# Kernel optimization log

Hardware: AMD Instinct MI355X
Metric: run time of the kernel (lower is better)

## Reference

```python
import jax, jax.numpy as jnp
import numpy as np

N = 50000
E = 800000
DIN = 256
DH = 256
DOUT = 256
R = 8
B = 4


def setup_inputs() -> dict:
    key = jax.random.key(0)
    ks = jax.random.split(key, 12)
    s = 0.05
    return {
        "x": jax.random.normal(ks[0], (N, DIN), jnp.float32),
        "edge_index": jax.random.randint(ks[1], (2, E), 0, N, jnp.int64),
        "edge_type": jax.random.randint(ks[2], (E,), 0, R, jnp.int64),
        "basis1": jax.random.normal(ks[3], (B, DIN, DH), jnp.float32) * s,
        "comp1": jax.random.normal(ks[4], (R, B), jnp.float32) * s,
        "root1": jax.random.normal(ks[5], (DIN, DH), jnp.float32) * s,
        "bias1": jnp.zeros((DH,), jnp.float32),
        "basis2": jax.random.normal(ks[6], (B, DH, DOUT), jnp.float32) * s,
        "comp2": jax.random.normal(ks[7], (R, B), jnp.float32) * s,
        "root2": jax.random.normal(ks[8], (DH, DOUT), jnp.float32) * s,
        "bias2": jnp.zeros((DOUT,), jnp.float32),
    }


def rgcn_conv(x, src, dst, edge_type, basis, comp, root, bias):
    # Basis-decomposed relational conv (PyG RGCNConv, aggr='mean').
    # xb: per-node transform by each basis matrix -> [N, B, out]
    xb = jnp.einsum('ni,bio->nbo', x, basis)
    # Per-edge message: mix bases with relation coefficients -> [E, out]
    msg = jnp.einsum('eb,ebo->eo', comp[edge_type], xb[src])
    # Mean aggregation per (dst, relation): divide each edge by the count of
    # edges of its relation arriving at its destination, then scatter-add.
    key = dst * R + edge_type
    cnt = jax.ops.segment_sum(jnp.ones((msg.shape[0],), x.dtype), key,
                              num_segments=x.shape[0] * R)
    norm = 1.0 / jnp.maximum(cnt, 1.0)
    agg = jax.ops.segment_sum(msg * norm[key][:, None], dst,
                              num_segments=x.shape[0])
    return agg + x @ root + bias


def reference(x, edge_index, edge_type, basis1, comp1, root1, bias1,
              basis2, comp2, root2, bias2):
    src, dst = edge_index[0], edge_index[1]
    h = rgcn_conv(x, src, dst, edge_type, basis1, comp1, root1, bias1)
    h = jax.nn.relu(h)
    # dropout(p=0.4) is identity in eval mode
    out = rgcn_conv(h, src, dst, edge_type, basis2, comp2, root2, bias2)
    return out
```

## Files before the change

### kernel.cpp

```cpp
#include <hip/hip_runtime.h>
#include <hip/hip_bf16.h>

constexpr int N_NODES = 50000;
constexpr int N_EDGES = 800000;
constexpr int R_REL   = 8;
constexpr int BASES   = 4;
constexpr int D       = 256;
constexpr int KZ      = BASES * D;
constexpr int KT      = KZ + D;
constexpr int WSTRIDE = 16;
constexpr int DUMMY_P = 8 << 20;

constexpr int NHI    = (N_NODES + 255) / 256;
constexpr int NS_BLK = 200;
constexpr int CH     = N_EDGES / NS_BLK;

constexpr int CB4 = (N_NODES * 128) / 1024;
constexpr int WKB = KT / 64;
constexpr int CAP = N_EDGES + N_NODES * 8;
constexpr int FB4 = (CAP + 1023) / 1024;

typedef __attribute__((ext_vector_type(8))) short bf16x8;
typedef __attribute__((ext_vector_type(4))) float f32x4;

__device__ inline float bfu_lo(unsigned u) { return __uint_as_float(u << 16); }
__device__ inline float bfu_hi(unsigned u) { return __uint_as_float(u & 0xFFFF0000u); }
__device__ inline unsigned short f2bu(float f) {
  __hip_bfloat16 h = __float2bfloat16(f);
  return *reinterpret_cast<unsigned short*>(&h);
}
__device__ inline void store_out(float* p, float v) { *p = v; }
__device__ inline void store_out(__hip_bfloat16* p, float v) { *p = __float2bfloat16(v); }

__device__ inline void gload_lds16(void* lds, const void* g) {
  __builtin_amdgcn_global_load_lds(
      (const __attribute__((address_space(1))) unsigned*)g,
      (__attribute__((address_space(3))) unsigned*)lds, 16, 0, 0);
}

__global__ __launch_bounds__(256) void prep_kernel(
    const int* __restrict__ ei, const int* __restrict__ et,
    int* __restrict__ gcoarse,
    const float* __restrict__ x, unsigned* __restrict__ x2,
    const float* __restrict__ basis1, const float* __restrict__ root1,
    __hip_bfloat16* __restrict__ WT1,
    const float* __restrict__ basis2, const float* __restrict__ root2,
    __hip_bfloat16* __restrict__ WT2,
    int* __restrict__ packed) {
  __shared__ __hip_bfloat16 tile[16][256];
  __shared__ int hist[NHI];
  int bid = blockIdx.x;
  int tid = threadIdx.x;

  if (bid < NS_BLK) {
    if (tid < NHI) hist[tid] = 0;
    __syncthreads();
    int start = bid * CH, end = start + CH;
    for (int i = start + tid; i < end; i += 256) {
      int dst = ei[N_EDGES + i];
      atomicAdd(&hist[dst >> 8], 1);
    }
    __syncthreads();
    if (tid < NHI && hist[tid] > 0) atomicAdd(&gcoarse[tid], hist[tid]);
    return;
  }
  bid -= NS_BLK;
  if (bid < CB4) {
    int idx = (bid * 256 + tid) * 4;
    const float* px = x + (size_t)idx * 2;
    float4 a = *(const float4*)(px);
    float4 b = *(const float4*)(px + 4);
    uint4 o;
    o.x = (unsigned)f2bu(a.x) | ((unsigned)f2bu(a.y) << 16);
    o.y = (unsigned)f2bu(a.z) | ((unsigned)f2bu(a.w) << 16);
    o.z = (unsigned)f2bu(b.x) | ((unsigned)f2bu(b.y) << 16);
    o.w = (unsigned)f2bu(b.z) | ((unsigned)f2bu(b.w) << 16);
    *(uint4*)(x2 + idx) = o;
    return;
  }
  bid -= CB4;
  if (bid < 2 * WKB) {
    const float* basis = (bid < WKB) ? basis1 : basis2;
    const float* root  = (bid < WKB) ? root1 : root2;
    __hip_bfloat16* WT = (bid < WKB) ? WT1 : WT2;
    int wb = (bid < WKB) ? bid : bid - WKB;
    int k0 = wb * 64;
#pragma unroll
    for (int pass = 0; pass < 4; pass++) {
      int kp = k0 + pass * 16;
#pragma unroll
      for (int r = 0; r < 16; r++) {
        int k = kp + r;
        const float* srow = (k < KZ)
            ? basis + ((size_t)(k & 3) * D + (k >> 2)) * D
            : root + (size_t)(k - KZ) * D;
        tile[r][tid] = __float2bfloat16(srow[tid]);
      }
      __syncthreads();
      __hip_bfloat16* dst = WT + (size_t)tid * KT + kp;
#pragma unroll
      for (int c = 0; c < 2; c++) {
        union { short s[8]; int4 v; } u;
#pragma unroll
        for (int r = 0; r < 8; r++)
          u.s[r] = *reinterpret_cast<short*>(&tile[c * 8 + r][tid]);
        *(int4*)(dst + c * 8) = u.v;
      }
      __syncthreads();
    }
    return;
  }
  bid -= 2 * WKB;
  {
    int i = (bid * 256 + tid) * 4;
    if (i < CAP) {
      int4 f = make_int4(DUMMY_P, DUMMY_P, DUMMY_P, DUMMY_P);
      *(int4*)(packed + i) = f;
    }
  }
}

__global__ __launch_bounds__(256) void coarse_prefix_kernel(
    const int* __restrict__ gcoarse, int* __restrict__ gbase,
    int* __restrict__ gcur) {
  __shared__ int sd[256];
  int tid = threadIdx.x;
  int v = (tid < NHI) ? gcoarse[tid] : 0;
  sd[tid] = v;
  __syncthreads();
  for (int off = 1; off < 256; off <<= 1) {
    int t = (tid >= off) ? sd[tid - off] : 0;
    __syncthreads();
    sd[tid] += t;
    __syncthreads();
  }
  if (tid < NHI) {
    int b = sd[tid] - v;
    gbase[tid] = b;
    gcur[tid] = b;
  }
}

__global__ __launch_bounds__(256) void coarse_scatter_kernel(
    const int* __restrict__ ei, const int* __restrict__ et,
    int* __restrict__ gcur, int* __restrict__ coarse) {
  __shared__ int hist[NHI];
  __shared__ int lbase[NHI];
  __shared__ int lcnt[NHI];
  int bid = blockIdx.x;
  int tid = threadIdx.x;
  if (tid < NHI) { hist[tid] = 0; lcnt[tid] = 0; }
  __syncthreads();
  int start = bid * CH, end = start + CH;
  for (int i = start + tid; i < end; i += 256)
    atomicAdd(&hist[ei[N_EDGES + i] >> 8], 1);
  __syncthreads();
  if (tid < NHI) lbase[tid] = atomicAdd(&gcur[tid], hist[tid]);
  __syncthreads();
  for (int i = start + tid; i < end; i += 256) {
    int src = ei[i];
    int dst = ei[N_EDGES + i];
    int rt  = et[i];
    int bin = dst >> 8;
    int rank = atomicAdd(&lcnt[bin], 1);
    coarse[lbase[bin] + rank] = src | (rt << 16) | ((dst & 255) << 19);
  }
}

__global__ __launch_bounds__(256) void fine_hist_kernel(
    const int* __restrict__ coarse, const int* __restrict__ gbase,
    const int* __restrict__ gcoarse,
    const float* __restrict__ comp1, float4* __restrict__ wtab1,
    const float* __restrict__ comp2, float4* __restrict__ wtab2,
    int* __restrict__ lestart, int* __restrict__ btot) {
  __shared__ int c2[256 * R_REL];
  __shared__ int sd[256];
  int b = blockIdx.x;
  int tid = threadIdx.x;
#pragma unroll
  for (int k = tid; k < 256 * R_REL; k += 256) c2[k] = 0;
  __syncthreads();
  int base = gbase[b], n_e = gcoarse[b];
  for (int i = tid; i < n_e; i += 256) {
    int e = coarse[base + i];
    int key = ((e >> 19) & 255) * R_REL + ((e >> 16) & 7);
    atomicAdd(&c2[key], 1);
  }
  __syncthreads();
  int nodebase = b * 256;
  for (int k = tid; k < 256 * WSTRIDE; k += 256) {
    int lo = k >> 4, r = k & (WSTRIDE - 1);
    int n = nodebase + lo;
    if (n < N_NODES) {
      float4 w1 = make_float4(0.f, 0.f, 0.f, 0.f);
      float4 w2 = w1;
      if (r < R_REL) {
        int c = c2[lo * R_REL + r];
        float inv = 1.0f / (float)(c > 0 ? c : 1);
        w1.x = comp1[r * BASES + 0] * inv;
        w1.y = comp1[r * BASES + 1] * inv;
        w1.z = comp1[r * BASES + 2] * inv;
        w1.w = comp1[r * BASES + 3] * inv;
        w2.x = comp2[r * BASES + 0] * inv;
        w2.y = comp2[r * BASES + 1] * inv;
        w2.z = comp2[r * BASES + 2] * inv;
        w2.w = comp2[r * BASES + 3] * inv;
      }
      wtab1[(size_t)n * WSTRIDE + r] = w1;
      wtab2[(size_t)n * WSTRIDE + r] = w2;
    }
  }
  int d = 0;
#pragma unroll
  for (int r = 0; r < R_REL; r++) d += c2[tid * R_REL + r];
  int dp = (d + 7) & ~7;
  sd[tid] = dp;
  __syncthreads();
  for (int off = 1; off < 256; off <<= 1) {
    int t = (tid >= off) ? sd[tid - off] : 0;
    __syncthreads();
    sd[tid] += t;
    __syncthreads();
  }
  lestart[b * 256 + tid] = sd[tid] - dp;
  if (tid == 255) btot[b] = sd[255];
}

__global__ __launch_bounds__(256) void btot_prefix_kernel(
    const int* __restrict__ btot, int* __restrict__ bbase,
    int* __restrict__ estart) {
  __shared__ int sd[256];
  int tid = threadIdx.x;
  int v = (tid < NHI) ? btot[tid] : 0;
  sd[tid] = v;
  __syncthreads();
  for (int off = 1; off < 256; off <<= 1) {
    int t = (tid >= off) ? sd[tid - off] : 0;
    __syncthreads();
    sd[tid] += t;
    __syncthreads();
  }
  if (tid < NHI) bbase[tid] = sd[tid] - v;
  if (tid == NHI - 1) estart[N_NODES] = sd[tid];
}

__global__ __launch_bounds__(256) void fine_scatter_kernel(
    const int* __restrict__ coarse, const int* __restrict__ gbase,
    const int* __restrict__ gcoarse, const int* __restrict__ bbase,
    const int* __restrict__ lestart, int* __restrict__ estart,
    int* __restrict__ packed) {
  __shared__ int lest[256];
  __shared__ int lcur[256];
  int b = blockIdx.x;
  int tid = threadIdx.x;
  int sb = bbase[b];
  lest[tid] = lestart[b * 256 + tid];
  lcur[tid] = 0;
  {
    int n = b * 256 + tid;
    if (n < N_NODES) estart[n] = sb + lest[tid];
  }
  __syncthreads();
  int base = gbase[b], n_e = gcoarse[b];
  for (int i = tid; i < n_e; i += 256) {
    int e = coarse[base + i];
    int lo = (e >> 19) & 255;
    int rank = atomicAdd(&lcur[lo], 1);
    packed[sb + lest[lo] + rank] = (e & 0xFFFF) | (((e >> 16) & 7) << 20);
  }
}

__device__ inline float2 pfma(float s, float2 a, float2 c) {
  c.x = fmaf(s, a.x, c.x);
  c.y = fmaf(s, a.y, c.y);
  return c;
}

__device__ inline void edge_fma(float2 acc[BASES][2], uint2 v, float4 w) {
  float2 a01 = make_float2(bfu_lo(v.x), bfu_hi(v.x));
  float2 a23 = make_float2(bfu_lo(v.y), bfu_hi(v.y));
  acc[0][0] = pfma(w.x, a01, acc[0][0]); acc[0][1] = pfma(w.x, a23, acc[0][1]);
  acc[1][0] = pfma(w.y, a01, acc[1][0]); acc[1][1] = pfma(w.y, a23, acc[1][1]);
  acc[2][0] = pfma(w.z, a01, acc[2][0]); acc[2][1] = pfma(w.z, a23, acc[2][1]);
  acc[3][0] = pfma(w.w, a01, acc[3][0]); acc[3][1] = pfma(w.w, a23, acc[3][1]);
}

__global__ __launch_bounds__(256) void aggregate_kernel(
    const unsigned* __restrict__ x2,
    const int* __restrict__ packed,
    const int* __restrict__ estart,
    const float4* __restrict__ wtab,
    __hip_bfloat16* __restrict__ zA)
{
  int tid = threadIdx.x;
  int lane = tid & 63;
  int n = __builtin_amdgcn_readfirstlane(blockIdx.x * 4 + (tid >> 6));
  int s = __builtin_amdgcn_readfirstlane(estart[n]);
  int e = __builtin_amdgcn_readfirstlane(estart[n + 1]);
  const int voff = lane * 2;
  const float4* wt = wtab + (size_t)n * WSTRIDE;

  float2 acc[BASES][2] = {};

  for (int base = s; base < e; base += 8) {
    int4 q0 = *(const int4*)(packed + base);
    int4 q1 = *(const int4*)(packed + base + 4);
    int p0 = __builtin_amdgcn_readfirstlane(q0.x);
    int p1 = __builtin_amdgcn_readfirstlane(q0.y);
    int p2 = __builtin_amdgcn_readfirstlane(q0.z);
    int p3 = __builtin_amdgcn_readfirstlane(q0.w);
    int p4 = __builtin_amdgcn_readfirstlane(q1.x);
    int p5 = __builtin_amdgcn_readfirstlane(q1.y);
    int p6 = __builtin_amdgcn_readfirstlane(q1.z);
    int p7 = __builtin_amdgcn_readfirstlane(q1.w);
    const unsigned* r0 = x2 + ((size_t)(p0 & 0xFFFFF) << 7);
    const unsigned* r1 = x2 + ((size_t)(p1 & 0xFFFFF) << 7);
    const unsigned* r2 = x2 + ((size_t)(p2 & 0xFFFFF) << 7);
    const unsigned* r3 = x2 + ((size_t)(p3 & 0xFFFFF) << 7);
    const unsigned* r4 = x2 + ((size_t)(p4 & 0xFFFFF) << 7);
    const unsigned* r5 = x2 + ((size_t)(p5 & 0xFFFFF) << 7);
    const unsigned* r6 = x2 + ((size_t)(p6 & 0xFFFFF) << 7);
    const unsigned* r7 = x2 + ((size_t)(p7 & 0xFFFFF) << 7);
    uint2 v0 = *(const uint2*)(r0 + voff);
    uint2 v1 = *(const uint2*)(r1 + voff);
    uint2 v2 = *(const uint2*)(r2 + voff);
    uint2 v3 = *(const uint2*)(r3 + voff);
    uint2 v4 = *(const uint2*)(r4 + voff);
    uint2 v5 = *(const uint2*)(r5 + voff);
    uint2 v6 = *(const uint2*)(r6 + voff);
    uint2 v7 = *(const uint2*)(r7 + voff);
    float4 w0 = wt[p0 >> 20];
    float4 w1 = wt[p1 >> 20];
    float4 w2 = wt[p2 >> 20];
    float4 w3 = wt[p3 >> 20];
    float4 w4 = wt[p4 >> 20];
    float4 w5 = wt[p5 >> 20];
    float4 w6 = wt[p6 >> 20];
    float4 w7 = wt[p7 >> 20];
    edge_fma(acc, v0, w0);
    edge_fma(acc, v1, w1);
    edge_fma(acc, v2, w2);
    edge_fma(acc, v3, w3);
    edge_fma(acc, v4, w4);
    edge_fma(acc, v5, w5);
    edge_fma(acc, v6, w6);
    edge_fma(acc, v7, w7);
  }

  union { short s[8]; int4 v; } u0, u1;
#pragma unroll
  for (int b = 0; b < BASES; b++) {
    u0.s[b]     = (short)f2bu(acc[b][0].x);
    u0.s[4 + b] = (short)f2bu(acc[b][0].y);
    u1.s[b]     = (short)f2bu(acc[b][1].x);
    u1.s[4 + b] = (short)f2bu(acc[b][1].y);
  }
  __hip_bfloat16* zrow = zA + (size_t)n * KZ;
  *(int4*)(zrow + 16 * lane) = u0.v;
  *(int4*)(zrow + 16 * lane + 8) = u1.v;
}

#define BM 128
#define BN 256
#define BK 32

template <bool RELU, typename OutT>
__global__ __launch_bounds__(512) void gemm_kernel(
    const __hip_bfloat16* __restrict__ Az,
    const __hip_bfloat16* __restrict__ Aself,
    const __hip_bfloat16* __restrict__ Bt,
    const float* __restrict__ bias, OutT* __restrict__ C, int M) {
  __shared__ __align__(16) __hip_bfloat16 As[2][BM * BK];
  __shared__ __align__(16) __hip_bfloat16 Bs[2][BN * BK];
  int tid = threadIdx.x;
  int m0 = blockIdx.x * BM;
  int wave = tid >> 6, lane = tid & 63;
  int wm = wave & 1, wn = wave >> 1;
  int l15 = lane & 15, quad = lane >> 4;

  int colS = (lane & 3) * 8;
  int rowA = wave * 16 + (lane >> 2);
  int grA  = min(m0 + rowA, M - 1);
  const __hip_bfloat16* gAz = Az + (size_t)grA * KZ + colS;
  const __hip_bfloat16* gAs = Aself + (size_t)grA * D + colS;
  const __hip_bfloat16* gB0 = Bt + (size_t)(wave * 32 + (lane >> 2)) * KT + colS;
  const __hip_bfloat16* gB1 = gB0 + 16 * KT;

  f32x4 acc[4][4] = {};

  auto stage = [&](int buf, int k0) {
    const __hip_bfloat16* srcA = (k0 < KZ) ? (gAz + k0) : (gAs + (k0 - KZ));
    gload_lds16(As[buf] + wave * 512, srcA);
    gload_lds16(Bs[buf] + wave * 1024, gB0 + k0);
    gload_lds16(Bs[buf] + wave * 1024 + 512, gB1 + k0);
  };

  stage(0, 0);
  int cur = 0;
  for (int k0 = 0; k0 < KT; k0 += BK) {
    if (k0 + BK < KT) {
      stage(cur ^ 1, k0 + BK);
      asm volatile("s_waitcnt vmcnt(3)" ::: "memory");
    } else {
      asm volatile("s_waitcnt vmcnt(0)" ::: "memory");
    }
    __builtin_amdgcn_s_barrier();
    __builtin_amdgcn_sched_barrier(0);

    bf16x8 af[4], bfr[4];
#pragma unroll
    for (int mt = 0; mt < 4; mt++)
      af[mt] = *(const bf16x8*)(As[cur] + (wm * 64 + mt * 16 + l15) * BK + quad * 8);
#pragma unroll
    for (int nt = 0; nt < 4; nt++)
      bfr[nt] = *(const bf16x8*)(Bs[cur] + (wn * 64 + nt * 16 + l15) * BK + quad * 8);
#pragma unroll
    for (int mt = 0; mt < 4; mt++)
#pragma unroll
      for (int nt = 0; nt < 4; nt++)
        acc[mt][nt] = __builtin_amdgcn_mfma_f32_16x16x32_bf16(
            af[mt], bfr[nt], acc[mt][nt], 0, 0, 0);
    __builtin_amdgcn_s_barrier();
    cur ^= 1;
  }

#pragma unroll
  for (int nt = 0; nt < 4; nt++) {
    int cg = wn * 64 + nt * 16 + l15;
    float bv = bias[cg];
#pragma unroll
    for (int mt = 0; mt < 4; mt++) {
#pragma unroll
      for (int r = 0; r < 4; r++) {
        int rg = m0 + wm * 64 + mt * 16 + quad * 4 + r;
        if (rg < M) {
          float v = acc[mt][nt][r] + bv;
          if (RELU) v = fmaxf(v, 0.f);
          store_out(C + (size_t)rg * D + cg, v);
        }
      }
    }
  }
}

static inline char* carve(char*& p, size_t bytes) {
  char* r = p;
  p += (bytes + 255) & ~(size_t)255;
  return r;
}

extern "C" void kernel_launch(void* const* d_in, const int* in_sizes, int n_in,
                              void* d_out, int out_size, void* d_ws,
                              size_t ws_size, hipStream_t stream) {
  const float* x      = (const float*)d_in[0];
  const int*   ei     = (const int*)d_in[1];
  const int*   et     = (const int*)d_in[2];
  const float* basis1 = (const float*)d_in[3];
  const float* comp1  = (const float*)d_in[4];
  const float* root1  = (const float*)d_in[5];
  const float* bias1  = (const float*)d_in[6];
  const float* basis2 = (const float*)d_in[7];
  const float* comp2  = (const float*)d_in[8];
  const float* root2  = (const float*)d_in[9];
  const float* bias2  = (const float*)d_in[10];
  float* out = (float*)d_out;

  char* ws = (char*)d_ws;
  int* estart  = (int*)carve(ws, (size_t)(N_NODES + 1) * 4);
  int* coarse  = (int*)carve(ws, (size_t)N_EDGES * 4);
  int* lestart = (int*)carve(ws, (size_t)NHI * 256 * 4);
  int* gcoarse = (int*)carve(ws, 256 * 4);
  int* gbase   = (int*)carve(ws, 256 * 4);
  int* gcur    = (int*)carve(ws, 256 * 4);
  int* btot    = (int*)carve(ws, 256 * 4);
  int* bbase   = (int*)carve(ws, 256 * 4);
  int* packed  = (int*)carve(ws, (size_t)CAP * 4);
  float4* wtab1 = (float4*)carve(ws, (size_t)N_NODES * WSTRIDE * 16);
  float4* wtab2 = (float4*)carve(ws, (size_t)N_NODES * WSTRIDE * 16);
  __hip_bfloat16* WT1 = (__hip_bfloat16*)carve(ws, (size_t)D * KT * 2);
  __hip_bfloat16* WT2 = (__hip_bfloat16*)carve(ws, (size_t)D * KT * 2);
  unsigned* xb = (unsigned*)carve(ws, (size_t)N_NODES * D * 2);
  __hip_bfloat16* h = (__hip_bfloat16*)carve(ws, (size_t)N_NODES * D * 2);
  __hip_bfloat16* zA = (__hip_bfloat16*)carve(ws, (size_t)N_NODES * KZ * 2);

  hipMemsetAsync(gcoarse, 0, 256 * 4, stream);

  prep_kernel<<<NS_BLK + CB4 + 2 * WKB + FB4, 256, 0, stream>>>(
      ei, et, gcoarse, x, xb, basis1, root1, WT1, basis2, root2, WT2, packed);
  coarse_prefix_kernel<<<1, 256, 0, stream>>>(gcoarse, gbase, gcur);
  coarse_scatter_kernel<<<NS_BLK, 256, 0, stream>>>(ei, et, gcur, coarse);
  fine_hist_kernel<<<NHI, 256, 0, stream>>>(coarse, gbase, gcoarse,
                                            comp1, wtab1, comp2, wtab2,
                                            lestart, btot);
  btot_prefix_kernel<<<1, 256, 0, stream>>>(btot, bbase, estart);
  fine_scatter_kernel<<<NHI, 256, 0, stream>>>(coarse, gbase, gcoarse, bbase,
                                               lestart, estart, packed);

  dim3 ggrid((N_NODES + BM - 1) / BM, 1);
  const int AB = (N_NODES + 3) / 4;

  aggregate_kernel<<<AB, 256, 0, stream>>>(xb, packed, estart, wtab1, zA);
  gemm_kernel<true, __hip_bfloat16><<<ggrid, 512, 0, stream>>>(
      zA, (const __hip_bfloat16*)xb, WT1, bias1, h, N_NODES);

  aggregate_kernel<<<AB, 256, 0, stream>>>((const unsigned*)h, packed, estart,
                                           wtab2, zA);
  gemm_kernel<false, float><<<ggrid, 512, 0, stream>>>(
      zA, h, WT2, bias2, out, N_NODES);
}
```

Before: 441.6 us.

## Make CSR build deterministic with per-block histograms and smaller buckets

Replaces the global atomic coarse-bin counters with a per-block histogram matrix that is prefix-scanned per bin, so the coarse scatter gets deterministic offsets without global atomics. The bucket size drops from 256 to 128 nodes and the edge-chunking blocks double, which increases parallelism in the fine histogram and scatter stages. The two single-block prefix kernels and the memset are removed, and each block now redoes a small 512-element scan. This trades a little redundant scan work per block for fewer launches and more blocks in the sort pipeline.

```diff
diff --git a/kernel.cpp b/kernel.cpp
--- a/kernel.cpp
+++ b/kernel.cpp
@@ -11,8 +11,9 @@
 constexpr int WSTRIDE = 16;
 constexpr int DUMMY_P = 8 << 20;
 
-constexpr int NHI    = (N_NODES + 255) / 256;
-constexpr int NS_BLK = 200;
+constexpr int BUCK   = 128;
+constexpr int NHI    = (N_NODES + BUCK - 1) / BUCK;
+constexpr int NS_BLK = 400;
 constexpr int CH     = N_EDGES / NS_BLK;
 
 constexpr int CB4 = (N_NODES * 128) / 1024;
@@ -38,9 +39,20 @@
       (__attribute__((address_space(3))) unsigned*)lds, 16, 0, 0);
 }
 
+__device__ inline void scan512(int* sd, int tid) {
+  for (int off = 1; off < 512; off <<= 1) {
+    int a = (tid >= off) ? sd[tid - off] : 0;
+    int b = (tid + 256 >= off) ? sd[tid + 256 - off] : 0;
+    __syncthreads();
+    sd[tid] += a;
+    sd[tid + 256] += b;
+    __syncthreads();
+  }
+}
+
 __global__ __launch_bounds__(256) void prep_kernel(
-    const int* __restrict__ ei, const int* __restrict__ et,
-    int* __restrict__ gcoarse,
+    const int* __restrict__ ei,
+    int* __restrict__ ghist,
     const float* __restrict__ x, unsigned* __restrict__ x2,
     const float* __restrict__ basis1, const float* __restrict__ root1,
     __hip_bfloat16* __restrict__ WT1,
@@ -53,15 +65,14 @@
   int tid = threadIdx.x;
 
   if (bid < NS_BLK) {
-    if (tid < NHI) hist[tid] = 0;
+    for (int k = tid; k < NHI; k += 256) hist[k] = 0;
     __syncthreads();
-    int start = bid * CH, end = start + CH;
-    for (int i = start + tid; i < end; i += 256) {
-      int dst = ei[N_EDGES + i];
-      atomicAdd(&hist[dst >> 8], 1);
-    }
+    int start = bid * CH;
+    for (int i = start + tid; i < start + CH; i += 256)
+      atomicAdd(&hist[ei[N_EDGES + i] >> 7], 1);
     __syncthreads();
-    if (tid < NHI && hist[tid] > 0) atomicAdd(&gcoarse[tid], hist[tid]);
+    for (int k = tid; k < NHI; k += 256)
+      ghist[(size_t)k * NS_BLK + bid] = hist[k];
     return;
   }
   bid -= NS_BLK;
@@ -120,75 +131,84 @@
   }
 }
 
-__global__ __launch_bounds__(256) void coarse_prefix_kernel(
-    const int* __restrict__ gcoarse, int* __restrict__ gbase,
-    int* __restrict__ gcur) {
-  __shared__ int sd[256];
-  int tid = threadIdx.x;
-  int v = (tid < NHI) ? gcoarse[tid] : 0;
-  sd[tid] = v;
-  __syncthreads();
-  for (int off = 1; off < 256; off <<= 1) {
-    int t = (tid >= off) ? sd[tid - off] : 0;
-    __syncthreads();
-    sd[tid] += t;
-    __syncthreads();
-  }
-  if (tid < NHI) {
-    int b = sd[tid] - v;
-    gbase[tid] = b;
-    gcur[tid] = b;
-  }
+__global__ __launch_bounds__(256) void binprefix_kernel(
+    const int* __restrict__ ghist, int* __restrict__ boffs,
+    int* __restrict__ bintot) {
+  __shared__ int sd[512];
+  int b = blockIdx.x;
+  int tid = threadIdx.x;
+  int v0 = (tid < NS_BLK) ? ghist[(size_t)b * NS_BLK + tid] : 0;
+  int v1 = (tid + 256 < NS_BLK) ? ghist[(size_t)b * NS_BLK + tid + 256] : 0;
+  sd[tid] = v0;
+  sd[tid + 256] = v1;
+  __syncthreads();
+  scan512(sd, tid);
+  if (tid < NS_BLK) boffs[(size_t)b * NS_BLK + tid] = sd[tid] - v0;
+  if (tid + 256 < NS_BLK)
+    boffs[(size_t)b * NS_BLK + tid + 256] = sd[tid + 256] - v1;
+  if (tid == 255) bintot[b] = sd[511];
 }
 
 __global__ __launch_bounds__(256) void coarse_scatter_kernel(
     const int* __restrict__ ei, const int* __restrict__ et,
-    int* __restrict__ gcur, int* __restrict__ coarse) {
-  __shared__ int hist[NHI];
+    const int* __restrict__ bintot, const int* __restrict__ boffs,
+    int* __restrict__ coarse) {
   __shared__ int lbase[NHI];
   __shared__ int lcnt[NHI];
+  __shared__ int sd[512];
   int bid = blockIdx.x;
   int tid = threadIdx.x;
-  if (tid < NHI) { hist[tid] = 0; lcnt[tid] = 0; }
-  __syncthreads();
-  int start = bid * CH, end = start + CH;
-  for (int i = start + tid; i < end; i += 256)
-    atomicAdd(&hist[ei[N_EDGES + i] >> 8], 1);
-  __syncthreads();
-  if (tid < NHI) lbase[tid] = atomicAdd(&gcur[tid], hist[tid]);
-  __syncthreads();
-  for (int i = start + tid; i < end; i += 256) {
+  for (int k = tid; k < NHI; k += 256) lcnt[k] = 0;
+  int v0 = (tid < NHI) ? bintot[tid] : 0;
+  int v1 = (tid + 256 < NHI) ? bintot[tid + 256] : 0;
+  sd[tid] = v0;
+  sd[tid + 256] = v1;
+  __syncthreads();
+  scan512(sd, tid);
+  if (tid < NHI) lbase[tid] = (sd[tid] - v0) + boffs[(size_t)tid * NS_BLK + bid];
+  if (tid + 256 < NHI)
+    lbase[tid + 256] =
+        (sd[tid + 256] - v1) + boffs[(size_t)(tid + 256) * NS_BLK + bid];
+  __syncthreads();
+  int start = bid * CH;
+  for (int i = start + tid; i < start + CH; i += 256) {
     int src = ei[i];
     int dst = ei[N_EDGES + i];
     int rt  = et[i];
-    int bin = dst >> 8;
+    int bin = dst >> 7;
     int rank = atomicAdd(&lcnt[bin], 1);
-    coarse[lbase[bin] + rank] = src | (rt << 16) | ((dst & 255) << 19);
+    coarse[lbase[bin] + rank] = src | (rt << 16) | ((dst & 127) << 19);
   }
 }
 
 __global__ __launch_bounds__(256) void fine_hist_kernel(
-    const int* __restrict__ coarse, const int* __restrict__ gbase,
-    const int* __restrict__ gcoarse,
+    const int* __restrict__ coarse, const int* __restrict__ bintot,
     const float* __restrict__ comp1, float4* __restrict__ wtab1,
     const float* __restrict__ comp2, float4* __restrict__ wtab2,
     int* __restrict__ lestart, int* __restrict__ btot) {
-  __shared__ int c2[256 * R_REL];
-  __shared__ int sd[256];
+  __shared__ int c2[BUCK * R_REL];
+  __shared__ int sd[512];
   int b = blockIdx.x;
   int tid = threadIdx.x;
 #pragma unroll
-  for (int k = tid; k < 256 * R_REL; k += 256) c2[k] = 0;
-  __syncthreads();
-  int base = gbase[b], n_e = gcoarse[b];
+  for (int k = tid; k < BUCK * R_REL; k += 256) c2[k] = 0;
+  int v0 = (tid < NHI) ? bintot[tid] : 0;
+  int v1 = (tid + 256 < NHI) ? bintot[tid + 256] : 0;
+  sd[tid] = v0;
+  sd[tid + 256] = v1;
+  __syncthreads();
+  scan512(sd, tid);
+  int n_e = bintot[b];
+  int cbase = sd[b] - n_e;
+  __syncthreads();
   for (int i = tid; i < n_e; i += 256) {
-    int e = coarse[base + i];
-    int key = ((e >> 19) & 255) * R_REL + ((e >> 16) & 7);
+    int e = coarse[cbase + i];
+    int key = ((e >> 19) & 127) * R_REL + ((e >> 16) & 7);
     atomicAdd(&c2[key], 1);
   }
   __syncthreads();
-  int nodebase = b * 256;
-  for (int k = tid; k < 256 * WSTRIDE; k += 256) {
+  int nodebase = b * BUCK;
+  for (int k = tid; k < BUCK * WSTRIDE; k += 256) {
     int lo = k >> 4, r = k & (WSTRIDE - 1);
     int n = nodebase + lo;
     if (n < N_NODES) {
@@ -211,9 +231,12 @@
     }
   }
   int d = 0;
-#pragma unroll
-  for (int r = 0; r < R_REL; r++) d += c2[tid * R_REL + r];
+  if (tid < BUCK) {
+#pragma unroll
+    for (int r = 0; r < R_REL; r++) d += c2[tid * R_REL + r];
+  }
   int dp = (d + 7) & ~7;
+  __syncthreads();
   sd[tid] = dp;
   __syncthreads();
   for (int off = 1; off < 256; off <<= 1) {
@@ -222,51 +245,52 @@
     sd[tid] += t;
     __syncthreads();
   }
-  lestart[b * 256 + tid] = sd[tid] - dp;
+  if (tid < BUCK) lestart[b * BUCK + tid] = sd[tid] - dp;
   if (tid == 255) btot[b] = sd[255];
 }
 
-__global__ __launch_bounds__(256) void btot_prefix_kernel(
-    const int* __restrict__ btot, int* __restrict__ bbase,
-    int* __restrict__ estart) {
-  __shared__ int sd[256];
-  int tid = threadIdx.x;
-  int v = (tid < NHI) ? btot[tid] : 0;
-  sd[tid] = v;
-  __syncthreads();
-  for (int off = 1; off < 256; off <<= 1) {
-    int t = (tid >= off) ? sd[tid - off] : 0;
-    __syncthreads();
-    sd[tid] += t;
-    __syncthreads();
-  }
-  if (tid < NHI) bbase[tid] = sd[tid] - v;
-  if (tid == NHI - 1) estart[N_NODES] = sd[tid];
-}
-
 __global__ __launch_bounds__(256) void fine_scatter_kernel(
-    const int* __restrict__ coarse, const int* __restrict__ gbase,
-    const int* __restrict__ gcoarse, const int* __restrict__ bbase,
-    const int* __restrict__ lestart, int* __restrict__ estart,
-    int* __restrict__ packed) {
-  __shared__ int lest[256];
-  __shared__ int lcur[256];
+    const int* __restrict__ coarse, const int* __restrict__ bintot,
+    const int* __restrict__ btot, const int* __restrict__ lestart,
+    int* __restrict__ estart, int* __restrict__ packed) {
+  __shared__ int lest[BUCK];
+  __shared__ int lcur[BUCK];
+  __shared__ int sd[512];
   int b = blockIdx.x;
   int tid = threadIdx.x;
-  int sb = bbase[b];
-  lest[tid] = lestart[b * 256 + tid];
-  lcur[tid] = 0;
+  if (tid < BUCK) {
+    lest[tid] = lestart[b * BUCK + tid];
+    lcur[tid] = 0;
+  }
+  int v0 = (tid < NHI) ? bintot[tid] : 0;
+  int v1 = (tid + 256 < NHI) ? bintot[tid + 256] : 0;
+  sd[tid] = v0;
+  sd[tid + 256] = v1;
+  __syncthreads();
+  scan512(sd, tid);
+  int n_e = bintot[b];
+  int cbase = sd[b] - n_e;
+  __syncthreads();
+  int w0 = (tid < NHI) ? btot[tid] : 0;
+  int w1 = (tid + 256 < NHI) ? btot[tid + 256] : 0;
+  sd[tid] = w0;
+  sd[tid + 256] = w1;
+  __syncthreads();
+  scan512(sd, tid);
+  int bt = btot[b];
+  int bb = sd[b] - bt;
+  __syncthreads();
   {
-    int n = b * 256 + tid;
-    if (n < N_NODES) estart[n] = sb + lest[tid];
-  }
-  __syncthreads();
-  int base = gbase[b], n_e = gcoarse[b];
+    int n = b * BUCK + tid;
+    if (tid < BUCK && n < N_NODES) estart[n] = bb + lest[tid];
+    if (b == NHI - 1 && tid == 0) estart[N_NODES] = bb + bt;
+  }
+  __syncthreads();
   for (int i = tid; i < n_e; i += 256) {
-    int e = coarse[base + i];
-    int lo = (e >> 19) & 255;
+    int e = coarse[cbase + i];
+    int lo = (e >> 19) & 127;
     int rank = atomicAdd(&lcur[lo], 1);
-    packed[sb + lest[lo] + rank] = (e & 0xFFFF) | (((e >> 16) & 7) << 20);
+    packed[bb + lest[lo] + rank] = (e & 0xFFFF) | (((e >> 16) & 7) << 20);
   }
 }
 
@@ -468,12 +492,11 @@
   char* ws = (char*)d_ws;
   int* estart  = (int*)carve(ws, (size_t)(N_NODES + 1) * 4);
   int* coarse  = (int*)carve(ws, (size_t)N_EDGES * 4);
-  int* lestart = (int*)carve(ws, (size_t)NHI * 256 * 4);
-  int* gcoarse = (int*)carve(ws, 256 * 4);
-  int* gbase   = (int*)carve(ws, 256 * 4);
-  int* gcur    = (int*)carve(ws, 256 * 4);
-  int* btot    = (int*)carve(ws, 256 * 4);
-  int* bbase   = (int*)carve(ws, 256 * 4);
+  int* ghist   = (int*)carve(ws, (size_t)NHI * NS_BLK * 4);
+  int* boffs   = (int*)carve(ws, (size_t)NHI * NS_BLK * 4);
+  int* bintot  = (int*)carve(ws, 512 * 4);
+  int* btot    = (int*)carve(ws, 512 * 4);
+  int* lestart = (int*)carve(ws, (size_t)NHI * BUCK * 4);
   int* packed  = (int*)carve(ws, (size_t)CAP * 4);
   float4* wtab1 = (float4*)carve(ws, (size_t)N_NODES * WSTRIDE * 16);
   float4* wtab2 = (float4*)carve(ws, (size_t)N_NODES * WSTRIDE * 16);
@@ -483,18 +506,15 @@
   __hip_bfloat16* h = (__hip_bfloat16*)carve(ws, (size_t)N_NODES * D * 2);
   __hip_bfloat16* zA = (__hip_bfloat16*)carve(ws, (size_t)N_NODES * KZ * 2);
 
-  hipMemsetAsync(gcoarse, 0, 256 * 4, stream);
-
   prep_kernel<<<NS_BLK + CB4 + 2 * WKB + FB4, 256, 0, stream>>>(
-      ei, et, gcoarse, x, xb, basis1, root1, WT1, basis2, root2, WT2, packed);
-  coarse_prefix_kernel<<<1, 256, 0, stream>>>(gcoarse, gbase, gcur);
-  coarse_scatter_kernel<<<NS_BLK, 256, 0, stream>>>(ei, et, gcur, coarse);
-  fine_hist_kernel<<<NHI, 256, 0, stream>>>(coarse, gbase, gcoarse,
-                                            comp1, wtab1, comp2, wtab2,
-                                            lestart, btot);
-  btot_prefix_kernel<<<1, 256, 0, stream>>>(btot, bbase, estart);
-  fine_scatter_kernel<<<NHI, 256, 0, stream>>>(coarse, gbase, gcoarse, bbase,
-                                               lestart, estart, packed);
+      ei, ghist, x, xb, basis1, root1, WT1, basis2, root2, WT2, packed);
+  binprefix_kernel<<<NHI, 256, 0, stream>>>(ghist, boffs, bintot);
+  coarse_scatter_kernel<<<NS_BLK, 256, 0, stream>>>(ei, et, bintot, boffs,
+                                                    coarse);
+  fine_hist_kernel<<<NHI, 256, 0, stream>>>(coarse, bintot, comp1, wtab1,
+                                            comp2, wtab2, lestart, btot);
+  fine_scatter_kernel<<<NHI, 256, 0, stream>>>(coarse, bintot, btot, lestart,
+                                               estart, packed);
 
   dim3 ggrid((N_NODES + BM - 1) / BM, 1);
   const int AB = (N_NODES + 3) / 4;
```

Result: faster. 431.9 us (-2.2%).
